# Kernel optimization log

Measured on AMD Instinct MI355X. Metric: run time of the kernel, lower is better.

The kernel has to match this reference:

```python
import jax, jax.numpy as jnp
import numpy as np

DEGREE = 8


def setup_inputs() -> dict:
    key = jax.random.key(0)
    k1, k2 = jax.random.split(key)
    x = jax.random.normal(k1, (8192, 1024), dtype=jnp.float32)
    # xavier_normal-ish scale for coeffs [input_dim, output_dim, degree+1]
    std = (2.0 / (1024 + 1024)) ** 0.5
    cheby_coeffs = jax.random.normal(k2, (1024, 1024, DEGREE + 1), dtype=jnp.float32) * std
    return {"x": x, "cheby_coeffs": cheby_coeffs}


def _cheby(x, degree):
    # x: [B, I] in [-1, 1]; returns T: [B, I, degree+1]
    T = [jnp.ones_like(x), x]
    for n in range(2, degree + 1):
        T.append(2.0 * x * T[-1] - T[-2])
    return jnp.stack(T, axis=-1)


def reference(x, cheby_coeffs) -> jnp.ndarray:
    input_dim = cheby_coeffs.shape[0]
    degree = cheby_coeffs.shape[-1] - 1
    x = x.reshape(-1, input_dim)
    xmin = jnp.min(x, axis=1, keepdims=True)
    xmax = jnp.max(x, axis=1, keepdims=True)
    x = 2.0 * (x - xmin) / (xmax - xmin) - 1.0
    T = _cheby(x, degree)  # [B, I, D+1]
    y = jnp.einsum('bij,ioj->bo', T, cheby_coeffs)
    return y
```

## Files before the change

### kernel.cpp

```cpp
#include <hip/hip_runtime.h>
#include <hip/hip_bf16.h>


typedef __attribute__((ext_vector_type(8))) short bf16x8s;
typedef __attribute__((ext_vector_type(4))) float f32x4;

constexpr int BROWS = 8192;
constexpr int IDIM  = 1024;
constexpr int ODIM  = 1024;
constexpr int DEG1  = 9;
constexpr int KP    = 8;
constexpr int KD    = IDIM * KP;

__device__ __forceinline__ ushort f2bf(float f) {
  return ((__hip_bfloat16_raw)__float2bfloat16(f)).x;
}

__device__ __forceinline__ void gload_lds16(const void* g, void* l) {
  __builtin_amdgcn_global_load_lds(
      (const __attribute__((address_space(1))) unsigned int*)g,
      (__attribute__((address_space(3))) unsigned int*)l, 16, 0, 0);
}

__global__ __launch_bounds__(256) void build_a_kernel(const float* __restrict__ x,
                                                      ushort* __restrict__ A2,
                                                      float* __restrict__ bias) {
  __shared__ float red[8];
  const int b = blockIdx.x, t = threadIdx.x, lane = t & 63, wv = t >> 6;
  if (b < 4) bias[b * 256 + t] = 0.0f;
  const float* xr = x + (size_t)b * IDIM;
  const float4 v = ((const float4*)xr)[t];
  float mn = fminf(fminf(v.x, v.y), fminf(v.z, v.w));
  float mx = fmaxf(fmaxf(v.x, v.y), fmaxf(v.z, v.w));
#pragma unroll
  for (int off = 32; off >= 1; off >>= 1) {
    mn = fminf(mn, __shfl_xor(mn, off));
    mx = fmaxf(mx, __shfl_xor(mx, off));
  }
  if (lane == 0) { red[wv] = mn; red[4 + wv] = mx; }
  __syncthreads();
  mn = fminf(fminf(red[0], red[1]), fminf(red[2], red[3]));
  mx = fmaxf(fmaxf(red[4], red[5]), fmaxf(red[6], red[7]));
  const float sc = 2.0f / (mx - mn);
  const float of = -mn * sc - 1.0f;

  uint4* adst = (uint4*)(A2 + (size_t)b * KD);
#pragma unroll
  for (int c = 0; c < 4; ++c) {
    const int i = c * 256 + t;
    const float xn = fmaf(sc, xr[i], of);
    const float T2 = 2.f * xn * xn - 1.f;
    const float T3 = 2.f * xn * T2 - xn;
    const float T4 = 2.f * xn * T3 - T2;
    const float T5 = 2.f * xn * T4 - T3;
    const float T6 = 2.f * xn * T5 - T4;
    const float T7 = 2.f * xn * T6 - T5;
    const float T8 = 2.f * xn * T7 - T6;
    uint4 w;
    w.x = (uint)f2bf(xn) | ((uint)f2bf(T2) << 16);
    w.y = (uint)f2bf(T3) | ((uint)f2bf(T4) << 16);
    w.z = (uint)f2bf(T5) | ((uint)f2bf(T6) << 16);
    w.w = (uint)f2bf(T7) | ((uint)f2bf(T8) << 16);
    adst[i] = w;
  }
}

__global__ __launch_bounds__(256) void build_b_kernel(const float* __restrict__ coeffs,
                                                      ushort* __restrict__ B2T,
                                                      float* __restrict__ bias) {
  __shared__ __align__(16) ushort tile[64 * 256];
  __shared__ float lb[64];
  const int i0 = blockIdx.x * 32;
  const int o0 = blockIdx.y * 64;
  const int t  = threadIdx.x;
  if (t < 64) lb[t] = 0.0f;
  __syncthreads();
  for (int idx = t; idx < 18432; idx += 256) {
    const int i_l = idx / 576;
    const int rem = idx - i_l * 576;
    const float v = coeffs[((size_t)(i0 + i_l) * ODIM + o0) * DEG1 + rem];
    const int o_l = rem / 9;
    const int j   = rem - o_l * 9;
    if (j == 0) atomicAdd(&lb[o_l], v);
    else tile[o_l * 256 + i_l * KP + (j - 1)] = f2bf(v);
  }
  __syncthreads();
  for (int idx = t; idx < 2048; idx += 256) {
    const int o_l = idx >> 5;
    const int w   = idx & 31;
    uint4* gdst = (uint4*)(B2T + (size_t)(o0 + o_l) * KD + i0 * KP);
    gdst[w] = ((const uint4*)tile)[idx];
  }
  if (t < 64) atomicAdd(&bias[o0 + t], lb[t]);
}

__global__ __launch_bounds__(256, 2) void gemm_kernel(const ushort* __restrict__ A2,
                                                      const ushort* __restrict__ B2T,
                                                      const float* __restrict__ bias,
                                                      float* __restrict__ out) {
  constexpr int BK    = 32;
  constexpr int KT    = KD / BK;
  constexpr int ABUF  = 256 * BK;
  constexpr int BBUF  = 64 * BK;
  constexpr int BUFSZ = ABUF + BBUF;
  __shared__ __align__(16) ushort Sm[3 * BUFSZ];

  const int t    = threadIdx.x;
  const int lane = t & 63;
  const int wave = t >> 6;
  const int c16  = lane & 15;
  const int quad = lane >> 4;

  const int orig = blockIdx.y * 16 + blockIdx.x;
  const int swz  = (orig & 7) * 64 + (orig >> 3);
  const int rowBase = (swz >> 4) * 256;
  const int colBase = (swz & 15) * 64;

  const int trow = t >> 2;
  const int scol = (t & 3) ^ ((t >> 3) & 3);
  const ushort* aB = A2  + (size_t)(rowBase + trow) * KD + scol * 8;
  const ushort* bB = B2T + (size_t)(colBase + trow) * KD + scol * 8;
  ushort* uS = Sm + t * 8;

  auto issA = [&](int buf, size_t ko, int a) {
    gload_lds16(aB + (size_t)a * (64 * KD) + ko, uS + buf * BUFSZ + a * 2048);
  };
  auto issB = [&](int buf, size_t ko) {
    gload_lds16(bB + ko, uS + buf * BUFSZ + ABUF);
  };

  const int cx   = (quad ^ ((c16 >> 1) & 3)) * 8;
  const int aoff = (wave * 64 + c16) * BK + cx;
  const int boff = c16 * BK + cx;

  f32x4 acc[4][4];
#pragma unroll
  for (int m = 0; m < 4; ++m)
#pragma unroll
    for (int n = 0; n < 4; ++n) acc[m][n] = (f32x4){0.f, 0.f, 0.f, 0.f};

  issA(0, 0, 0); issA(0, 0, 1); issA(0, 0, 2); issA(0, 0, 3); issB(0, 0);
  issA(1, BK, 0); issA(1, BK, 1); issA(1, BK, 2); issA(1, BK, 3); issB(1, BK);
  asm volatile("s_waitcnt vmcnt(5)" ::: "memory");
  __builtin_amdgcn_s_barrier();

  int cur = 0;
  for (int it = 0; it < KT; ++it) {
    const ushort* Asb = Sm + cur * BUFSZ;
    const ushort* Bsb = Asb + ABUF;
    const int nb = (cur >= 1) ? cur - 1 : 2;
    const size_t ko = (size_t)(it + 2) * BK;
    const bool pf = (it < KT - 2);

    bf16x8s afr[4], bfr[4];
#pragma unroll
    for (int m = 0; m < 4; ++m)
      afr[m] = *(const bf16x8s*)&Asb[aoff + m * (16 * BK)];
#pragma unroll
    for (int n = 0; n < 4; ++n)
      bfr[n] = *(const bf16x8s*)&Bsb[boff + n * (16 * BK)];

    if (pf) { issA(nb, ko, 0); issA(nb, ko, 1); issA(nb, ko, 2); issA(nb, ko, 3);
              issB(nb, ko); }

    __builtin_amdgcn_s_setprio(1);
#pragma unroll
    for (int m = 0; m < 4; ++m)
#pragma unroll
      for (int n = 0; n < 4; ++n)
        acc[m][n] = __builtin_amdgcn_mfma_f32_16x16x32_bf16(afr[m], bfr[n],
                                                            acc[m][n], 0, 0, 0);
    __builtin_amdgcn_s_setprio(0);

    if (pf)              { asm volatile("s_waitcnt vmcnt(5)" ::: "memory"); }
    else if (it == KT-2) { asm volatile("s_waitcnt vmcnt(0)" ::: "memory"); }
    __builtin_amdgcn_s_barrier();

    cur = (cur == 2) ? 0 : cur + 1;
  }

#pragma unroll
  for (int n = 0; n < 4; ++n) {
    const int col = colBase + n * 16 + c16;
    const float bv = bias[col];
#pragma unroll
    for (int m = 0; m < 4; ++m) {
      const int r0 = rowBase + wave * 64 + m * 16 + quad * 4;
#pragma unroll
      for (int r = 0; r < 4; ++r)
        out[(size_t)(r0 + r) * ODIM + col] = acc[m][n][r] + bv;
    }
  }
}

extern "C" void kernel_launch(void* const* d_in, const int* in_sizes, int n_in,
                              void* d_out, int out_size, void* d_ws, size_t ws_size,
                              hipStream_t stream) {
  const float* x      = (const float*)d_in[0];
  const float* coeffs = (const float*)d_in[1];
  float* out = (float*)d_out;

  char* ws = (char*)d_ws;
  float*  bias = (float*)ws;
  ushort* B2T  = (ushort*)(ws + 65536);
  ushort* A2   = (ushort*)(ws + 65536 + (size_t)ODIM * KD * 2);

  build_a_kernel<<<BROWS, 256, 0, stream>>>(x, A2, bias);
  build_b_kernel<<<dim3(IDIM / 32, ODIM / 64), 256, 0, stream>>>(coeffs, B2T, bias);
  gemm_kernel<<<dim3(ODIM / 64, BROWS / 256), 256, 0, stream>>>(A2, B2T, bias, out);
}
```

Baseline: 334.6 us.

## Enlarge GEMM block tile to 256x128 with 2x2 wave layout

Widens each GEMM workgroup's output tile from 256x64 to 256x128 and arranges the four waves as 2x2, each computing a 128x64 sub-tile with 8x4 MFMA accumulators. The intent is to raise arithmetic intensity and cut redundant global/LDS reads of the A operand, since each A tile now serves twice as many columns. The cost is 128 accumulator floats per thread plus more fragment registers, which may squeeze the requested 2 waves/SIMD occupancy. The grid shrinks to 256 blocks, which could underfill the GPU's compute units.

```diff
diff --git a/kernel.cpp b/kernel.cpp
--- a/kernel.cpp
+++ b/kernel.cpp
@@ -100,79 +100,88 @@
                                                       float* __restrict__ out) {
   constexpr int BK    = 32;
   constexpr int KT    = KD / BK;
-  constexpr int ABUF  = 256 * BK;
-  constexpr int BBUF  = 64 * BK;
-  constexpr int BUFSZ = ABUF + BBUF;
+  constexpr int ABUFU = 256 * BK;
+  constexpr int BBUFU = 128 * BK;
+  constexpr int BUFSZ = ABUFU + BBUFU;
   __shared__ __align__(16) ushort Sm[3 * BUFSZ];
 
   const int t    = threadIdx.x;
   const int lane = t & 63;
   const int wave = t >> 6;
+  const int wr   = wave >> 1;
+  const int wc   = wave & 1;
   const int c16  = lane & 15;
   const int quad = lane >> 4;
 
-  const int orig = blockIdx.y * 16 + blockIdx.x;
-  const int swz  = (orig & 7) * 64 + (orig >> 3);
-  const int rowBase = (swz >> 4) * 256;
-  const int colBase = (swz & 15) * 64;
+  const int orig = blockIdx.y * 8 + blockIdx.x;
+  const int swz  = (orig & 7) * 32 + (orig >> 3);
+  const int rowBase = (swz >> 3) * 256;
+  const int colBase = (swz & 7) * 128;
 
   const int trow = t >> 2;
   const int scol = (t & 3) ^ ((t >> 3) & 3);
   const ushort* aB = A2  + (size_t)(rowBase + trow) * KD + scol * 8;
   const ushort* bB = B2T + (size_t)(colBase + trow) * KD + scol * 8;
-  ushort* uS = Sm + t * 8;
-
-  auto issA = [&](int buf, size_t ko, int a) {
-    gload_lds16(aB + (size_t)a * (64 * KD) + ko, uS + buf * BUFSZ + a * 2048);
+  ushort* uA = Sm + t * 8;
+  ushort* uB = Sm + ABUFU + t * 8;
+
+  auto issA = [&](int buf, int itile, int a) {
+    gload_lds16(aB + (size_t)a * (64 * KD) + (size_t)itile * BK,
+                uA + buf * BUFSZ + a * 2048);
   };
-  auto issB = [&](int buf, size_t ko) {
-    gload_lds16(bB + ko, uS + buf * BUFSZ + ABUF);
+  auto issB = [&](int buf, int itile, int b2) {
+    gload_lds16(bB + (size_t)b2 * (64 * KD) + (size_t)itile * BK,
+                uB + buf * BUFSZ + b2 * 2048);
   };
 
   const int cx   = (quad ^ ((c16 >> 1) & 3)) * 8;
-  const int aoff = (wave * 64 + c16) * BK + cx;
-  const int boff = c16 * BK + cx;
-
-  f32x4 acc[4][4];
-#pragma unroll
-  for (int m = 0; m < 4; ++m)
+  const int aoff = (wr * 128 + c16) * BK + cx;
+  const int boff = (wc * 64 + c16) * BK + cx;
+
+  f32x4 acc[8][4];
+#pragma unroll
+  for (int m = 0; m < 8; ++m)
 #pragma unroll
     for (int n = 0; n < 4; ++n) acc[m][n] = (f32x4){0.f, 0.f, 0.f, 0.f};
 
-  issA(0, 0, 0); issA(0, 0, 1); issA(0, 0, 2); issA(0, 0, 3); issB(0, 0);
-  issA(1, BK, 0); issA(1, BK, 1); issA(1, BK, 2); issA(1, BK, 3); issB(1, BK);
-  asm volatile("s_waitcnt vmcnt(5)" ::: "memory");
+  issA(0, 0, 0); issA(0, 0, 1); issA(0, 0, 2); issA(0, 0, 3);
+  issB(0, 0, 0); issB(0, 0, 1);
+  issA(1, 1, 0); issA(1, 1, 1); issA(1, 1, 2); issA(1, 1, 3);
+  issB(1, 1, 0); issB(1, 1, 1);
+  asm volatile("s_waitcnt vmcnt(6)" ::: "memory");
   __builtin_amdgcn_s_barrier();
 
   int cur = 0;
   for (int it = 0; it < KT; ++it) {
     const ushort* Asb = Sm + cur * BUFSZ;
-    const ushort* Bsb = Asb + ABUF;
+    const ushort* Bsb = Asb + ABUFU;
     const int nb = (cur >= 1) ? cur - 1 : 2;
-    const size_t ko = (size_t)(it + 2) * BK;
     const bool pf = (it < KT - 2);
 
-    bf16x8s afr[4], bfr[4];
-#pragma unroll
-    for (int m = 0; m < 4; ++m)
+    bf16x8s afr[8], bfr[4];
+#pragma unroll
+    for (int m = 0; m < 8; ++m)
       afr[m] = *(const bf16x8s*)&Asb[aoff + m * (16 * BK)];
 #pragma unroll
     for (int n = 0; n < 4; ++n)
       bfr[n] = *(const bf16x8s*)&Bsb[boff + n * (16 * BK)];
 
-    if (pf) { issA(nb, ko, 0); issA(nb, ko, 1); issA(nb, ko, 2); issA(nb, ko, 3);
-              issB(nb, ko); }
+    if (pf) {
+      issA(nb, it + 2, 0); issA(nb, it + 2, 1);
+      issA(nb, it + 2, 2); issA(nb, it + 2, 3);
+      issB(nb, it + 2, 0); issB(nb, it + 2, 1);
+    }
 
     __builtin_amdgcn_s_setprio(1);
 #pragma unroll
-    for (int m = 0; m < 4; ++m)
+    for (int m = 0; m < 8; ++m)
 #pragma unroll
       for (int n = 0; n < 4; ++n)
         acc[m][n] = __builtin_amdgcn_mfma_f32_16x16x32_bf16(afr[m], bfr[n],
                                                             acc[m][n], 0, 0, 0);
     __builtin_amdgcn_s_setprio(0);
 
-    if (pf)              { asm volatile("s_waitcnt vmcnt(5)" ::: "memory"); }
+    if (pf)              { asm volatile("s_waitcnt vmcnt(6)" ::: "memory"); }
     else if (it == KT-2) { asm volatile("s_waitcnt vmcnt(0)" ::: "memory"); }
     __builtin_amdgcn_s_barrier();
 
@@ -181,11 +190,11 @@
 
 #pragma unroll
   for (int n = 0; n < 4; ++n) {
-    const int col = colBase + n * 16 + c16;
+    const int col = colBase + wc * 64 + n * 16 + c16;
     const float bv = bias[col];
 #pragma unroll
-    for (int m = 0; m < 4; ++m) {
-      const int r0 = rowBase + wave * 64 + m * 16 + quad * 4;
+    for (int m = 0; m < 8; ++m) {
+      const int r0 = rowBase + wr * 128 + m * 16 + quad * 4;
 #pragma unroll
       for (int r = 0; r < 4; ++r)
         out[(size_t)(r0 + r) * ODIM + col] = acc[m][n][r] + bv;
@@ -207,5 +216,5 @@
 
   build_a_kernel<<<BROWS, 256, 0, stream>>>(x, A2, bias);
   build_b_kernel<<<dim3(IDIM / 32, ODIM / 64), 256, 0, stream>>>(coeffs, B2T, bias);
-  gemm_kernel<<<dim3(ODIM / 64, BROWS / 256), 256, 0, stream>>>(A2, B2T, bias, out);
-}
+  gemm_kernel<<<dim3(ODIM / 128, BROWS / 256), 256, 0, stream>>>(A2, B2T, bias, out);
+}
```

Measured after the change: 297.5 us. 1.12x faster.

## Use 256x256 GEMM tiles with split-K over two groups and atomic output

Applied to the files above, without the earlier changes.

Rewrites the GEMM to 512-thread blocks computing 256x256 output tiles, with each wave holding a 128x64 accumulator. K is split into two halves whose partial sums are combined with atomicAdd into an output that build_a_kernel now zeroes. The main loop becomes a macro-unrolled four-phase pipeline that double-buffers 64-wide K slabs in LDS. The larger tiles raise data reuse per LDS load, and split-K keeps the grid at 256 blocks. In exchange it costs atomic traffic on every output element, extra zeroing writes, and higher register pressure from 32 accumulators.

```diff
diff --git a/kernel.cpp b/kernel.cpp
--- a/kernel.cpp
+++ b/kernel.cpp
@@ -11,6 +11,7 @@
 constexpr int DEG1  = 9;
 constexpr int KP    = 8;
 constexpr int KD    = IDIM * KP;
+constexpr int KH    = KD / 2;
 
 __device__ __forceinline__ ushort f2bf(float f) {
   return ((__hip_bfloat16_raw)__float2bfloat16(f)).x;
@@ -24,10 +25,12 @@
 
 __global__ __launch_bounds__(256) void build_a_kernel(const float* __restrict__ x,
                                                       ushort* __restrict__ A2,
-                                                      float* __restrict__ bias) {
+                                                      float* __restrict__ bias,
+                                                      float* __restrict__ out) {
   __shared__ float red[8];
   const int b = blockIdx.x, t = threadIdx.x, lane = t & 63, wv = t >> 6;
   if (b < 4) bias[b * 256 + t] = 0.0f;
+  ((float4*)(out + (size_t)b * ODIM))[t] = (float4){0.f, 0.f, 0.f, 0.f};
   const float* xr = x + (size_t)b * IDIM;
   const float4 v = ((const float4*)xr)[t];
   float mn = fminf(fminf(v.x, v.y), fminf(v.z, v.w));
@@ -94,101 +97,112 @@
   if (t < 64) atomicAdd(&bias[o0 + t], lb[t]);
 }
 
-__global__ __launch_bounds__(256, 2) void gemm_kernel(const ushort* __restrict__ A2,
+#define PHASE(SA, SB, MO, READ_B, STAGE_STMT, TAIL_STMT)                        \
+  {                                                                             \
+    const ushort* Ap = Sm + (SA) * 8192;                                        \
+    _Pragma("unroll")                                                           \
+    for (int mi = 0; mi < 4; ++mi)                                              \
+      afr[mi] = *(const bf16x8s*)&Ap[abase + ((MO) + mi) * 512];                \
+    if (READ_B) {                                                               \
+      const ushort* Bp = Sm + (SB) * 8192;                                      \
+      _Pragma("unroll")                                                         \
+      for (int ni = 0; ni < 4; ++ni)                                            \
+        bfr[ni] = *(const bf16x8s*)&Bp[bbase + ni * 512];                       \
+    }                                                                           \
+    STAGE_STMT;                                                                 \
+    __builtin_amdgcn_s_barrier();                                               \
+    asm volatile("s_waitcnt lgkmcnt(0)" ::: "memory");                          \
+    __builtin_amdgcn_s_setprio(1);                                              \
+    _Pragma("unroll")                                                           \
+    for (int mi = 0; mi < 4; ++mi)                                              \
+      _Pragma("unroll")                                                         \
+      for (int ni = 0; ni < 4; ++ni)                                            \
+        acc[(MO) + mi][ni] = __builtin_amdgcn_mfma_f32_16x16x32_bf16(           \
+            afr[mi], bfr[ni], acc[(MO) + mi][ni], 0, 0, 0);                     \
+    __builtin_amdgcn_s_setprio(0);                                              \
+    TAIL_STMT;                                                                  \
+    __builtin_amdgcn_s_barrier();                                               \
+  }
+
+#define TILE(T, P)                                                              \
+  {                                                                             \
+    const int ko = (T) * 64;                                                    \
+    PHASE((P)*4 + 0, (P)*4 + 2, 0, true,                                        \
+          if ((T) + 1 < KT) { stage(((P)^1)*4 + 1, aBs, ko + 96); }, ;)         \
+    PHASE((P)*4 + 0, (P)*4 + 2, 4, false,                                       \
+          if ((T) + 1 < KT) { stage(((P)^1)*4 + 3, bBs, ko + 96); }, ;)         \
+    PHASE((P)*4 + 1, (P)*4 + 3, 0, true,                                        \
+          if ((T) + 2 < KT) { stage((P)*4 + 0, aBs, ko + 128); }, ;)            \
+    PHASE((P)*4 + 1, (P)*4 + 3, 4, false,                                       \
+          if ((T) + 2 < KT) { stage((P)*4 + 2, bBs, ko + 128); },               \
+          if ((T) < KT - 2) { asm volatile("s_waitcnt vmcnt(4)" ::: "memory"); }\
+          else              { asm volatile("s_waitcnt vmcnt(0)" ::: "memory"); })\
+  }
+
+__global__ __launch_bounds__(512, 2) void gemm_kernel(const ushort* __restrict__ A2,
                                                       const ushort* __restrict__ B2T,
                                                       const float* __restrict__ bias,
                                                       float* __restrict__ out) {
-  constexpr int BK    = 32;
-  constexpr int KT    = KD / BK;
-  constexpr int ABUF  = 256 * BK;
-  constexpr int BBUF  = 64 * BK;
-  constexpr int BUFSZ = ABUF + BBUF;
-  __shared__ __align__(16) ushort Sm[3 * BUFSZ];
+  constexpr int KT = KH / 64;
+  __shared__ __align__(16) ushort Sm[8 * 8192];
 
   const int t    = threadIdx.x;
   const int lane = t & 63;
   const int wave = t >> 6;
+  const int wr   = wave >> 2;
+  const int wc   = wave & 3;
   const int c16  = lane & 15;
   const int quad = lane >> 4;
 
-  const int orig = blockIdx.y * 16 + blockIdx.x;
-  const int swz  = (orig & 7) * 64 + (orig >> 3);
-  const int rowBase = (swz >> 4) * 256;
-  const int colBase = (swz & 15) * 64;
+  const int orig = blockIdx.y * 4 + blockIdx.x;
+  const int swz  = (orig & 7) * 32 + (orig >> 3);
+  const int rowBase = (swz >> 3) * 256;
+  const int rem     = swz & 7;
+  const int colBase = (rem & 3) * 256;
+  const int g       = rem >> 2;
 
   const int trow = t >> 2;
   const int scol = (t & 3) ^ ((t >> 3) & 3);
-  const ushort* aB = A2  + (size_t)(rowBase + trow) * KD + scol * 8;
-  const ushort* bB = B2T + (size_t)(colBase + trow) * KD + scol * 8;
-  ushort* uS = Sm + t * 8;
-
-  auto issA = [&](int buf, size_t ko, int a) {
-    gload_lds16(aB + (size_t)a * (64 * KD) + ko, uS + buf * BUFSZ + a * 2048);
+  const ushort* aBs = A2  + (size_t)(rowBase + trow) * KD + (size_t)g * KH + scol * 8;
+  const ushort* bBs = B2T + (size_t)(colBase + trow) * KD + (size_t)g * KH + scol * 8;
+
+  auto stage = [&](int slot, const ushort* base, int koff) {
+    gload_lds16(base + koff,                 Sm + slot * 8192 + t * 8);
+    gload_lds16(base + (size_t)128 * KD + koff, Sm + slot * 8192 + 4096 + t * 8);
   };
-  auto issB = [&](int buf, size_t ko) {
-    gload_lds16(bB + ko, uS + buf * BUFSZ + ABUF);
-  };
-
-  const int cx   = (quad ^ ((c16 >> 1) & 3)) * 8;
-  const int aoff = (wave * 64 + c16) * BK + cx;
-  const int boff = c16 * BK + cx;
-
-  f32x4 acc[4][4];
-#pragma unroll
-  for (int m = 0; m < 4; ++m)
+
+  const int cx    = (quad ^ ((c16 >> 1) & 3)) * 8;
+  const int abase = (wr * 128 + c16) * 32 + cx;
+  const int bbase = (wc * 64 + c16) * 32 + cx;
+
+  f32x4 acc[8][4];
+#pragma unroll
+  for (int m = 0; m < 8; ++m)
 #pragma unroll
     for (int n = 0; n < 4; ++n) acc[m][n] = (f32x4){0.f, 0.f, 0.f, 0.f};
 
-  issA(0, 0, 0); issA(0, 0, 1); issA(0, 0, 2); issA(0, 0, 3); issB(0, 0);
-  issA(1, BK, 0); issA(1, BK, 1); issA(1, BK, 2); issA(1, BK, 3); issB(1, BK);
-  asm volatile("s_waitcnt vmcnt(5)" ::: "memory");
+  stage(0, aBs, 0);   stage(2, bBs, 0);
+  stage(1, aBs, 32);  stage(3, bBs, 32);
+  stage(4, aBs, 64);  stage(6, bBs, 64);
+  asm volatile("s_waitcnt vmcnt(4)" ::: "memory");
   __builtin_amdgcn_s_barrier();
 
-  int cur = 0;
-  for (int it = 0; it < KT; ++it) {
-    const ushort* Asb = Sm + cur * BUFSZ;
-    const ushort* Bsb = Asb + ABUF;
-    const int nb = (cur >= 1) ? cur - 1 : 2;
-    const size_t ko = (size_t)(it + 2) * BK;
-    const bool pf = (it < KT - 2);
-
-    bf16x8s afr[4], bfr[4];
-#pragma unroll
-    for (int m = 0; m < 4; ++m)
-      afr[m] = *(const bf16x8s*)&Asb[aoff + m * (16 * BK)];
-#pragma unroll
-    for (int n = 0; n < 4; ++n)
-      bfr[n] = *(const bf16x8s*)&Bsb[boff + n * (16 * BK)];
-
-    if (pf) { issA(nb, ko, 0); issA(nb, ko, 1); issA(nb, ko, 2); issA(nb, ko, 3);
-              issB(nb, ko); }
-
-    __builtin_amdgcn_s_setprio(1);
-#pragma unroll
-    for (int m = 0; m < 4; ++m)
-#pragma unroll
-      for (int n = 0; n < 4; ++n)
-        acc[m][n] = __builtin_amdgcn_mfma_f32_16x16x32_bf16(afr[m], bfr[n],
-                                                            acc[m][n], 0, 0, 0);
-    __builtin_amdgcn_s_setprio(0);
-
-    if (pf)              { asm volatile("s_waitcnt vmcnt(5)" ::: "memory"); }
-    else if (it == KT-2) { asm volatile("s_waitcnt vmcnt(0)" ::: "memory"); }
-    __builtin_amdgcn_s_barrier();
-
-    cur = (cur == 2) ? 0 : cur + 1;
-  }
-
-#pragma unroll
-  for (int n = 0; n < 4; ++n) {
-    const int col = colBase + n * 16 + c16;
-    const float bv = bias[col];
-#pragma unroll
-    for (int m = 0; m < 4; ++m) {
-      const int r0 = rowBase + wave * 64 + m * 16 + quad * 4;
+  bf16x8s afr[4], bfr[4];
+  for (int tb = 0; tb < KT; tb += 2) {
+    TILE(tb, 0)
+    TILE(tb + 1, 1)
+  }
+
+#pragma unroll
+  for (int ni = 0; ni < 4; ++ni) {
+    const int col = colBase + wc * 64 + ni * 16 + c16;
+    const float bv = (g == 0) ? bias[col] : 0.0f;
+#pragma unroll
+    for (int mi = 0; mi < 8; ++mi) {
+      const int r0 = rowBase + wr * 128 + mi * 16 + quad * 4;
 #pragma unroll
       for (int r = 0; r < 4; ++r)
-        out[(size_t)(r0 + r) * ODIM + col] = acc[m][n][r] + bv;
+        atomicAdd(&out[(size_t)(r0 + r) * ODIM + col], acc[mi][ni][r] + bv);
     }
   }
 }
@@ -205,7 +219,7 @@
   ushort* B2T  = (ushort*)(ws + 65536);
   ushort* A2   = (ushort*)(ws + 65536 + (size_t)ODIM * KD * 2);
 
-  build_a_kernel<<<BROWS, 256, 0, stream>>>(x, A2, bias);
+  build_a_kernel<<<BROWS, 256, 0, stream>>>(x, A2, bias, out);
   build_b_kernel<<<dim3(IDIM / 32, ODIM / 64), 256, 0, stream>>>(coeffs, B2T, bias);
-  gemm_kernel<<<dim3(ODIM / 64, BROWS / 256), 256, 0, stream>>>(A2, B2T, bias, out);
-}
+  gemm_kernel<<<dim3(4, 64), 512, 0, stream>>>(A2, B2T, bias, out);
+}
```

After: 312.0 us. 6.8% less time.
